# Performance work log

Hardware: AMD Instinct MI355X
Metric: run time of the kernel (lower is better)

## Reference

```python
import jax, jax.numpy as jnp
import numpy as np

B, C, M, NH, F_, W = 2, 8, 8, 8, 1024, 512  # batch, channels, attention_maps, heads, features, frames
HD = F_ // NH
EXP = 4


def _conv(x, w, b):
    y = jax.lax.conv_general_dilated(x, w, (1, 1), 'SAME',
                                     dimension_numbers=('NCHW', 'OIHW', 'NCHW'))
    return y + b[None, :, None, None]


def _rope(x):
    # x: (..., seq, d); lucidrains-style interleaved rotary embedding
    d, n = x.shape[-1], x.shape[-2]
    inv = 1.0 / (10000.0 ** (jnp.arange(0, d, 2, dtype=jnp.float32) / d))
    fr = jnp.repeat(jnp.arange(n, dtype=jnp.float32)[:, None] * inv[None, :], 2, axis=-1)
    cos, sin = jnp.cos(fr), jnp.sin(fr)
    xr = jnp.stack((-x[..., 1::2], x[..., 0::2]), axis=-1).reshape(x.shape)
    return x * cos + xr * sin


def _mcln(x, w, b, eps=1e-5):
    # MultichannelLayerNorm: normalize over features axis (axis=2 of B,C,F,W)
    mu = jnp.mean(x, axis=2, keepdims=True)
    var = jnp.var(x, axis=2, keepdims=True)
    return (x - mu) / jnp.sqrt(var + eps) * w[None, :, :, None] + b[None, :, :, None]


def _mclin(x, w_pw):
    # MultichannelLinear positionwise: per-channel matmul over features
    return jnp.einsum('bcfw,cgf->bcgw', x, w_pw)


def setup_inputs() -> dict:
    key = jax.random.key(0)
    ks = jax.random.split(key, 24)
    s = 0.02
    d = {
        'x': jax.random.normal(ks[0], (B, C, F_, W), jnp.float32),
        'prev_qk': jax.random.normal(ks[1], (B, M, NH, W, W), jnp.float32),
        'qconv_w': jax.random.normal(ks[2], (M, C, 3, 3), jnp.float32) * s,
        'qconv_b': jnp.zeros((M,), jnp.float32),
        'q_pw': jax.random.normal(ks[3], (M, F_, F_), jnp.float32) * s,
        'kconv_w': jax.random.normal(ks[4], (M, C, 3, 3), jnp.float32) * s,
        'kconv_b': jnp.zeros((M,), jnp.float32),
        'k_pw': jax.random.normal(ks[5], (M, F_, F_), jnp.float32) * s,
        'vconv_w': jax.random.normal(ks[6], (M, C, 3, 3), jnp.float32) * s,
        'vconv_b': jnp.zeros((M,), jnp.float32),
        'v_pw': jax.random.normal(ks[7], (M, F_, F_), jnp.float32) * s,
        'o_pw': jax.random.normal(ks[8], (M, F_, F_), jnp.float32) * s,
        'o_dw': jax.random.normal(ks[9], (M, M), jnp.float32) * s,
        'oproj_w': jax.random.normal(ks[10], (C, C + M, 3, 3), jnp.float32) * s,
        'oproj_b': jnp.zeros((C,), jnp.float32),
        'n1_w': jnp.ones((C, F_), jnp.float32),
        'n1_b': jnp.zeros((C, F_), jnp.float32),
        'c1_w': jax.random.normal(ks[11], (C * EXP, C, 3, 3), jnp.float32) * s,
        'c1_b': jnp.zeros((C * EXP,), jnp.float32),
        'c2_w': jax.random.normal(ks[12], (C, C * EXP, 3, 3), jnp.float32) * s,
        'c2_b': jnp.zeros((C,), jnp.float32),
        'n2_w': jnp.ones((C, F_), jnp.float32),
        'n2_b': jnp.zeros((C, F_), jnp.float32),
    }
    return d


def _encoder(x, prev_qk, qconv_w, qconv_b, q_pw, kconv_w, kconv_b, k_pw,
             vconv_w, vconv_b, v_pw, o_pw, o_dw, oproj_w, oproj_b,
             n1_w, n1_b, c1_w, c1_b, c2_w, c2_b, n2_w, n2_b):
    b, c, h, w = x.shape

    def heads(y):  # (B,M,F,W) -> (B,M,NH,W,HD)
        return y.transpose(0, 1, 3, 2).reshape(b, M, w, NH, HD).transpose(0, 1, 3, 2, 4)

    q = _rope(heads(_mclin(_conv(x, qconv_w, qconv_b), q_pw)))
    k = _rope(heads(_mclin(_conv(x, kconv_w, kconv_b), k_pw)))
    v = heads(_mclin(_conv(x, vconv_w, vconv_b), v_pw))

    qk = jnp.einsum('bmnqd,bmnkd->bmnqk', q, k) / jnp.sqrt(jnp.float32(h))
    qk = qk + prev_qk
    a = jnp.einsum('bmnqk,bmnkd->bmnqd', jax.nn.softmax(qk, axis=-1), v)
    a = a.transpose(0, 1, 3, 2, 4).reshape(b, M, w, NH * HD).transpose(0, 1, 3, 2)  # (B,M,F,W)
    a = jnp.einsum('bcfw,dc->bdfw', _mclin(a, o_pw), o_dw)  # depthwise o_linear
    z = _conv(jnp.concatenate((x, a), axis=1), oproj_w, oproj_b)

    hid = _mcln(x + z, n1_w, n1_b)  # dropout is identity in eval
    z2 = _conv(jax.nn.gelu(_conv(hid, c1_w, c1_b), approximate=False), c2_w, c2_b)
    out = _mcln(hid + z2, n2_w, n2_b)
    return out, qk


def reference(x, prev_qk, qconv_w, qconv_b, q_pw, kconv_w, kconv_b, k_pw,
              vconv_w, vconv_b, v_pw, o_pw, o_dw, oproj_w, oproj_b,
              n1_w, n1_b, c1_w, c1_b, c2_w, c2_b, n2_w, n2_b):
    out, qk = _encoder(x, prev_qk, qconv_w, qconv_b, q_pw, kconv_w, kconv_b, k_pw,
                       vconv_w, vconv_b, v_pw, o_pw, o_dw, oproj_w, oproj_b,
                       n1_w, n1_b, c1_w, c1_b, c2_w, c2_b, n2_w, n2_b)
    return (out, out, qk)
```

## Files before the change

### kernel.cpp

```cpp
#include <hip/hip_runtime.h>
#include <math.h>

#define B_ 2
#define C_ 8
#define M_ 8
#define NH_ 8
#define F_ 1024
#define W_ 512
#define HD_ 128
#define FW 524288L
#define PF_ 1026
#define PW_ 514

typedef __bf16 bf16_t;
typedef __bf16 bf16x8 __attribute__((ext_vector_type(8)));
typedef __bf16 bf16x4 __attribute__((ext_vector_type(4)));
typedef float f32x4 __attribute__((ext_vector_type(4)));

__device__ __forceinline__ void gload16(const void* g, void* l) {
    __builtin_amdgcn_global_load_lds(
        (const __attribute__((address_space(1))) unsigned int*)g,
        (__attribute__((address_space(3))) unsigned int*)l,
        16, 0, 0);
}

__device__ __forceinline__ float gelu_f(float v) {
    return 0.5f * v * (1.0f + erff(v * 0.70710678118f));
}

__device__ __forceinline__ void xcd_swz3(int& bx, int& by, int& bz) {
    const int nwg = gridDim.x * gridDim.y * gridDim.z;
    int orig = blockIdx.x + gridDim.x * (blockIdx.y + gridDim.y * blockIdx.z);
    orig = (orig & 7) * (nwg >> 3) + (orig >> 3);
    bx = orig % gridDim.x;
    int t = orig / gridDim.x;
    by = t % gridDim.y;
    bz = t / gridDim.y;
}

__global__ __launch_bounds__(256)
void prep_k(const float* __restrict__ q_pw, const float* __restrict__ k_pw,
            const float* __restrict__ v_pw, const float* __restrict__ o_pw,
            const float* __restrict__ x,
            const float* __restrict__ qw, const float* __restrict__ kw,
            const float* __restrict__ vw, const float* __restrict__ ow,
            const float* __restrict__ c1w, const float* __restrict__ c2w,
            const float* __restrict__ qb, const float* __restrict__ kb,
            const float* __restrict__ vb,
            bf16_t* __restrict__ W4, bf16_t* __restrict__ px,
            bf16_t* __restrict__ a_qkv, bf16_t* __restrict__ a_op,
            bf16_t* __restrict__ a_c1, bf16_t* __restrict__ a_c2,
            float* __restrict__ bias_qkv,
            bf16_t* __restrict__ p8a, bf16_t* __restrict__ p8b, bf16_t* __restrict__ p32)
{
    const int bid = blockIdx.x, tid = threadIdx.x;
    if (bid < 32768) {
        long i = (long)bid * 256 + tid;
        const int wsel = (int)(i >> 21);
        const long off = i & 2097151L;
        const float* src = (wsel == 0) ? q_pw : (wsel == 1) ? k_pw : (wsel == 2) ? v_pw : o_pw;
        float4 v = ((const float4*)src)[off];
        bf16x4 r = { (bf16_t)v.x, (bf16_t)v.y, (bf16_t)v.z, (bf16_t)v.w };
        *(bf16x4*)&W4[i * 4] = r;
    } else if (bid < 36889) {
        long i = (long)(bid - 32768) * 256 + tid;
        if (i >= (long)B_ * PF_ * PW_) return;
        int wc = (int)(i % PW_);
        long t = i / PW_;
        int fr = (int)(t % PF_);
        int b  = (int)(t / PF_);
        bf16x8 v = {};
        if (fr >= 1 && fr <= F_ && wc >= 1 && wc <= W_) {
            const float* s = x + (long)b * 8 * FW + (long)(fr - 1) * W_ + (wc - 1);
            #pragma unroll
            for (int c = 0; c < 8; ++c) v[c] = (bf16_t)s[c * FW];
        }
        *(bf16x8*)&px[i * 8] = v;
    } else if (bid < 36961) {
        int sub = bid - 36889;
        int mode = sub / 18;
        int i = (sub % 18) * 256 + tid;
        if (mode == 0) {
            if (i < 3072) {
                int k = i & 31, co = (i >> 5) & 31, df = i >> 10;
                int tap = k >> 3, ci = k & 7;
                float v = 0.f;
                if (tap < 3) {
                    if (co < 8)       v = qw[((co * 8 + ci) * 3 + df) * 3 + tap];
                    else if (co < 16) v = kw[(((co - 8) * 8 + ci) * 3 + df) * 3 + tap];
                    else if (co < 24) v = vw[(((co - 16) * 8 + ci) * 3 + df) * 3 + tap];
                }
                a_qkv[i] = (bf16_t)v;
            }
            if (i < 32) bias_qkv[i] = (i < 8) ? qb[i] : (i < 16) ? kb[i - 8] : (i < 24) ? vb[i - 16] : 0.f;
        } else if (mode == 1) {
            if (i < 3072) {
                int k = i & 63, co = (i >> 6) & 15, df = i >> 10;
                int src = k >> 5, r = k & 31, tap = r >> 3, ci = src * 8 + (r & 7);
                float v = 0.f;
                if (co < 8 && tap < 3) v = ow[((co * 16 + ci) * 3 + df) * 3 + tap];
                a_op[i] = (bf16_t)v;
            }
        } else if (mode == 2) {
            if (i < 3072) {
                int k = i & 31, co = (i >> 5) & 31, df = i >> 10;
                int tap = k >> 3, ci = k & 7;
                float v = (tap < 3) ? c1w[((co * 8 + ci) * 3 + df) * 3 + tap] : 0.f;
                a_c1[i] = (bf16_t)v;
            }
        } else {
            if (i < 4608) {
                int k = i % 96, co = (i / 96) & 15, df = i / (96 * 16);
                int tap = k >> 5, ci = k & 31;
                float v = (co < 8) ? c2w[((co * 32 + ci) * 3 + df) * 3 + tap] : 0.f;
                a_c2[i] = (bf16_t)v;
            }
        }
    } else {
        int i = (bid - 36961) * 256 + tid;
        if (i >= 2 * 3076) return;
        int b = i / 3076, p = i % 3076;
        int fr, wc;
        if (p < 514)       { fr = 0;    wc = p; }
        else if (p < 1028) { fr = 1025; wc = p - 514; }
        else if (p < 2052) { fr = 1 + (p - 1028); wc = 0; }
        else               { fr = 1 + (p - 2052); wc = 513; }
        long pix = ((long)b * PF_ + fr) * PW_ + wc;
        bf16x8 z = {};
        *(bf16x8*)&p8a[pix * 8] = z;
        *(bf16x8*)&p8b[pix * 8] = z;
        #pragma unroll
        for (int k = 0; k < 4; ++k) *(bf16x8*)&p32[pix * 32 + k * 8] = z;
    }
}

template<int CIN, int KSTEPS, int MFRAGS, int DUAL, int EPI, int RESBF>
__global__ __launch_bounds__(256)
void convg_k(const bf16_t* __restrict__ px0, const bf16_t* __restrict__ px1,
             const bf16_t* __restrict__ Ab, const float* __restrict__ bias,
             const void* __restrict__ resid, void* __restrict__ outp)
{
    const int f = blockIdx.y, b = blockIdx.z;
    const int tid = threadIdx.x, lane = tid & 63, wid = tid >> 6;
    const int l15 = lane & 15, l4 = lane >> 4;
    const int wbase = blockIdx.x * 256 + wid * 64;
    const int KW = KSTEPS * 32, M16 = MFRAGS * 16;

    bf16x8 af[3][MFRAGS][KSTEPS];
    #pragma unroll
    for (int df = 0; df < 3; ++df)
        #pragma unroll
        for (int mf = 0; mf < MFRAGS; ++mf)
            #pragma unroll
            for (int kk = 0; kk < KSTEPS; ++kk)
                af[df][mf][kk] = *(const bf16x8*)&Ab[(long)(df * M16 + mf * 16 + l15) * KW + kk * 32 + l4 * 8];

    f32x4 acc[MFRAGS][4];
    #pragma unroll
    for (int mf = 0; mf < MFRAGS; ++mf)
        #pragma unroll
        for (int nf = 0; nf < 4; ++nf)
            acc[mf][nf] = (f32x4){0.f, 0.f, 0.f, 0.f};

    #pragma unroll
    for (int df = 0; df < 3; ++df) {
        const long rowb = ((long)(b * PF_ + f + df)) * PW_ * CIN;
        #pragma unroll
        for (int nf = 0; nf < 4; ++nf) {
            const int wp = wbase + nf * 16 + l15;
            #pragma unroll
            for (int kk = 0; kk < KSTEPS; ++kk) {
                const bf16_t* src = (DUAL && kk == 1) ? px1 : px0;
                long addr = (CIN == 8) ? rowb + (long)(wp + l4) * 8
                                       : rowb + (long)(wp + kk) * 32 + l4 * 8;
                bf16x8 bv = *(const bf16x8*)&src[addr];
                #pragma unroll
                for (int mf = 0; mf < MFRAGS; ++mf)
                    acc[mf][nf] = __builtin_amdgcn_mfma_f32_16x16x32_bf16(
                        af[df][mf][kk], bv, acc[mf][nf], 0, 0, 0);
            }
        }
    }

    #pragma unroll
    for (int mf = 0; mf < MFRAGS; ++mf) {
        #pragma unroll
        for (int nf = 0; nf < 4; ++nf) {
            const int wp = wbase + nf * 16 + l15;
            if (EPI == 2) {
                const int cob = mf * 16 + l4 * 4;
                bf16x4 ov;
                #pragma unroll
                for (int r = 0; r < 4; ++r)
                    ov[r] = (bf16_t)gelu_f(acc[mf][nf][r] + bias[cob + r]);
                *(bf16x4*)&((bf16_t*)outp)[(((long)(b * PF_ + f + 1)) * PW_ + wp + 1) * 32 + cob] = ov;
            } else {
                #pragma unroll
                for (int r = 0; r < 4; ++r) {
                    const int co = mf * 16 + l4 * 4 + r;
                    float v = acc[mf][nf][r];
                    if (EPI == 0) {
                        if (co < 24)
                            ((bf16_t*)outp)[((long)(b * 24 + co)) * FW + (long)f * W_ + wp] = (bf16_t)(v + bias[co]);
                    } else {
                        if (co < 8) {
                            long oi = ((long)(b * 8 + co)) * FW + (long)f * W_ + wp;
                            float rv = RESBF ? (float)((const bf16_t*)resid)[oi]
                                             : ((const float*)resid)[oi];
                            ((bf16_t*)outp)[oi] = (bf16_t)(v + bias[co] + rv);
                        }
                    }
                }
            }
        }
    }
}

template<int OUTBF>
__global__ __launch_bounds__(256, 4)
void gemm_mfma_k(const bf16_t* __restrict__ Ab, const bf16_t* __restrict__ Bb,
                 void* __restrict__ Cb,
                 int Kdim, int lda, int ldb, int ldc,
                 long sA, long sB, long sC_hi, long sC_lo, int zdivC, int aMod)
{
    __shared__ bf16_t sAt[8192];
    __shared__ bf16_t sBt[8192];

    int bx, by, bz;
    xcd_swz3(bx, by, bz);
    const int z = bz;
    const int m0 = by * 128;
    const int n0 = bx * 128;
    const int tid = threadIdx.x;
    const int lane = tid & 63, wid = tid >> 6;
    const int wr = (wid >> 1) * 64, wc = (wid & 1) * 64;
    const int l15 = lane & 15, l4 = lane >> 4;

    const bf16_t* A = Ab + (long)(z % aMod) * sA;
    const bf16_t* B = Bb + (long)z * sB;

    f32x4 acc[4][4];
    #pragma unroll
    for (int m = 0; m < 4; ++m)
        #pragma unroll
        for (int n = 0; n < 4; ++n)
            acc[m][n] = (f32x4){0.f, 0.f, 0.f, 0.f};

    const int grow = wid * 8 + (lane >> 3);
    const int gslot = lane & 7;

    for (int k0 = 0; k0 < Kdim; k0 += 64) {
        __syncthreads();
        #pragma unroll
        for (int r = 0; r < 4; ++r) {
            const int row = r * 32 + grow;
            gload16(A + (long)(m0 + row) * lda + k0 + ((gslot ^ (row & 7)) << 3),
                    sAt + r * 2048 + wid * 512);
        }
        #pragma unroll
        for (int r = 0; r < 4; ++r) {
            const int row = r * 32 + grow;
            gload16(B + (long)(n0 + row) * ldb + k0 + ((gslot ^ (row & 7)) << 3),
                    sBt + r * 2048 + wid * 512);
        }
        __syncthreads();

        bf16x8 afr[4][2], bfr[4][2];
        #pragma unroll
        for (int m = 0; m < 4; ++m) {
            const int row = wr + m * 16 + l15, swz = row & 7;
            afr[m][0] = *(const bf16x8*)&sAt[row * 64 + ((l4 ^ swz) << 3)];
            afr[m][1] = *(const bf16x8*)&sAt[row * 64 + (((4 + l4) ^ swz) << 3)];
        }
        #pragma unroll
        for (int n = 0; n < 4; ++n) {
            const int row = wc + n * 16 + l15, swz = row & 7;
            bfr[n][0] = *(const bf16x8*)&sBt[row * 64 + ((l4 ^ swz) << 3)];
            bfr[n][1] = *(const bf16x8*)&sBt[row * 64 + (((4 + l4) ^ swz) << 3)];
        }
        #pragma unroll
        for (int kk = 0; kk < 2; ++kk)
            #pragma unroll
            for (int m = 0; m < 4; ++m)
                #pragma unroll
                for (int n = 0; n < 4; ++n)
                    acc[m][n] = __builtin_amdgcn_mfma_f32_16x16x32_bf16(
                        afr[m][kk], bfr[n][kk], acc[m][n], 0, 0, 0);
    }

    const long zc = (long)(z / zdivC) * sC_hi + (long)(z % zdivC) * sC_lo;
    #pragma unroll
    for (int m = 0; m < 4; ++m) {
        #pragma unroll
        for (int n = 0; n < 4; ++n) {
            #pragma unroll
            for (int r = 0; r < 4; ++r) {
                int row = m0 + wr + m * 16 + l4 * 4 + r;
                int col = n0 + wc + n * 16 + l15;
                float v = acc[m][n][r];
                long cidx = zc + (long)row * ldc + col;
                if (OUTBF) ((bf16_t*)Cb)[cidx] = (bf16_t)v;
                else       ((float*)Cb)[cidx]  = v;
            }
        }
    }
}

__global__ __launch_bounds__(256, 4)
void qkvgemm_k(const bf16_t* __restrict__ W4, const bf16_t* __restrict__ XT,
               bf16_t* __restrict__ outp )
{
    __shared__ bf16_t sAt[8192];
    __shared__ bf16_t sBt[8192];

    int bx, by, bz;
    xcd_swz3(bx, by, bz);
    const int zz = bz;
    const int path = zz >> 4, bm = zz & 15;
    const bf16_t* A = W4 + (long)(path * 8 + (bm & 7)) * 1048576L;
    const bf16_t* B = XT + (long)zz * FW;
    const int m0 = by * 128;
    const int n0 = bx * 128;
    const int tid = threadIdx.x;
    const int lane = tid & 63, wid = tid >> 6;
    const int wr = (wid >> 1) * 64, wc = (wid & 1) * 64;
    const int l15 = lane & 15, l4 = lane >> 4;

    f32x4 acc[4][4];
    #pragma unroll
    for (int m = 0; m < 4; ++m)
        #pragma unroll
        for (int n = 0; n < 4; ++n)
            acc[m][n] = (f32x4){0.f, 0.f, 0.f, 0.f};

    const int grow = wid * 8 + (lane >> 3);
    const int gslot = lane & 7;

    for (int k0 = 0; k0 < 1024; k0 += 64) {
        __syncthreads();
        #pragma unroll
        for (int r = 0; r < 4; ++r) {
            const int row = r * 32 + grow;
            gload16(A + (long)(m0 + row) * 1024 + k0 + ((gslot ^ (row & 7)) << 3),
                    sAt + r * 2048 + wid * 512);
        }
        #pragma unroll
        for (int r = 0; r < 4; ++r) {
            const int row = r * 32 + grow;
            gload16(B + (long)(n0 + row) * 1024 + k0 + ((gslot ^ (row & 7)) << 3),
                    sBt + r * 2048 + wid * 512);
        }
        __syncthreads();

        bf16x8 afr[4][2], bfr[4][2];
        #pragma unroll
        for (int m = 0; m < 4; ++m) {
            const int row = wr + m * 16 + l15, swz = row & 7;
            afr[m][0] = *(const bf16x8*)&sAt[row * 64 + ((l4 ^ swz) << 3)];
            afr[m][1] = *(const bf16x8*)&sAt[row * 64 + (((4 + l4) ^ swz) << 3)];
        }
        #pragma unroll
        for (int n = 0; n < 4; ++n) {
            const int row = wc + n * 16 + l15, swz = row & 7;
            bfr[n][0] = *(const bf16x8*)&sBt[row * 64 + ((l4 ^ swz) << 3)];
            bfr[n][1] = *(const bf16x8*)&sBt[row * 64 + (((4 + l4) ^ swz) << 3)];
        }
        #pragma unroll
        for (int kk = 0; kk < 2; ++kk)
            #pragma unroll
            for (int m = 0; m < 4; ++m)
                #pragma unroll
                for (int n = 0; n < 4; ++n)
                    acc[m][n] = __builtin_amdgcn_mfma_f32_16x16x32_bf16(
                        afr[m][kk], bfr[n][kk], acc[m][n], 0, 0, 0);
    }

    if (path < 2) {
        const long base = (long)path * 8388608L + (((long)bm * 8 + by) * 512L) * 128L;
        #pragma unroll
        for (int m = 0; m < 4; ++m) {
            const int d0 = wr + m * 16 + l4 * 4;
            const float inv0 = __expf(-(float)(d0 >> 1) * 0.14391156507f);
            const float inv1 = __expf(-(float)((d0 >> 1) + 1) * 0.14391156507f);
            #pragma unroll
            for (int n = 0; n < 4; ++n) {
                const int col = n0 + wc + n * 16 + l15;
                float s0, c0, s1, c1;
                __sincosf((float)col * inv0, &s0, &c0);
                __sincosf((float)col * inv1, &s1, &c1);
                float v0 = acc[m][n][0], v1 = acc[m][n][1];
                float v2 = acc[m][n][2], v3 = acc[m][n][3];
                bf16x4 ov = { (bf16_t)(v0 * c0 - v1 * s0), (bf16_t)(v1 * c0 + v0 * s0),
                              (bf16_t)(v2 * c1 - v3 * s1), (bf16_t)(v3 * c1 + v2 * s1) };
                *(bf16x4*)&outp[base + (long)col * 128 + d0] = ov;
            }
        }
    } else {
        const long base = 16777216L + (long)bm * FW;
        #pragma unroll
        for (int m = 0; m < 4; ++m)
            #pragma unroll
            for (int n = 0; n < 4; ++n)
                #pragma unroll
                for (int r = 0; r < 4; ++r) {
                    int row = m0 + wr + m * 16 + l4 * 4 + r;
                    int col = n0 + wc + n * 16 + l15;
                    outp[base + (long)row * 512 + col] = (bf16_t)acc[m][n][r];
                }
    }
}

__global__ __launch_bounds__(256, 4)
void attn_k(const bf16_t* __restrict__ QR, const bf16_t* __restrict__ KR,
            const bf16_t* __restrict__ VL, const float* __restrict__ prevb,
            float* __restrict__ Sout, bf16_t* __restrict__ AT)
{
    __shared__ bf16_t sA[4096];
    __shared__ bf16_t sB[8192];
    __shared__ float red[2][64][2];
    __shared__ float Mrun[64], Srun[64];

    int bx, by, bz;
    xcd_swz3(bx, by, bz);
    (void)by;
    const int z = bz;
    const int m0 = bx * 64;
    const bf16_t* Qb = QR + (long)z * 65536L;
    const bf16_t* Kb = KR + (long)z * 65536L;
    const bf16_t* Vb = VL + (long)z * 65536L;
    const float* prev = prevb + (long)z * 262144L;
    float* Sb = Sout + (long)z * 262144L;

    const int tid = threadIdx.x, lane = tid & 63, wid = tid >> 6;
    const int l15 = lane & 15, l4 = lane >> 4;
    const int wr = (wid >> 1) * 32, wc = (wid & 1) * 64;
    const int grow = wid * 8 + (lane >> 3);
    const int gslot = lane & 7;

    if (tid < 64) { Mrun[tid] = -1e30f; Srun[tid] = 0.f; }

    for (int kc = 0; kc < 4; ++kc) {
        f32x4 acc[2][4];
        #pragma unroll
        for (int m = 0; m < 2; ++m)
            #pragma unroll
            for (int n = 0; n < 4; ++n)
                acc[m][n] = (f32x4){0.f, 0.f, 0.f, 0.f};

        #pragma unroll
        for (int k0 = 0; k0 < 128; k0 += 64) {
            __syncthreads();
            #pragma unroll
            for (int r = 0; r < 2; ++r) {
                const int row = r * 32 + grow;
                gload16(Qb + (long)(m0 + row) * 128 + k0 + ((gslot ^ (row & 7)) << 3),
                        sA + r * 2048 + wid * 512);
            }
            #pragma unroll
            for (int r = 0; r < 4; ++r) {
                const int row = r * 32 + grow;
                gload16(Kb + (long)(kc * 128 + row) * 128 + k0 + ((gslot ^ (row & 7)) << 3),
                        sB + r * 2048 + wid * 512);
            }
            __syncthreads();

            bf16x8 afr[2][2], bfr[4][2];
            #pragma unroll
            for (int m = 0; m < 2; ++m) {
                const int row = wr + m * 16 + l15, swz = row & 7;
                afr[m][0] = *(const bf16x8*)&sA[row * 64 + ((l4 ^ swz) << 3)];
                afr[m][1] = *(const bf16x8*)&sA[row * 64 + (((4 + l4) ^ swz) << 3)];
            }
            #pragma unroll
            for (int n = 0; n < 4; ++n) {
                const int row = wc + n * 16 + l15, swz = row & 7;
                bfr[n][0] = *(const bf16x8*)&sB[row * 64 + ((l4 ^ swz) << 3)];
                bfr[n][1] = *(const bf16x8*)&sB[row * 64 + (((4 + l4) ^ swz) << 3)];
            }
            __builtin_amdgcn_s_setprio(1);
            #pragma unroll
            for (int kk = 0; kk < 2; ++kk)
                #pragma unroll
                for (int m = 0; m < 2; ++m)
                    #pragma unroll
                    for (int n = 0; n < 4; ++n)
                        acc[m][n] = __builtin_amdgcn_mfma_f32_16x16x32_bf16(
                            afr[m][kk], bfr[n][kk], acc[m][n], 0, 0, 0);
            __builtin_amdgcn_s_setprio(0);
        }

        #pragma unroll
        for (int m = 0; m < 2; ++m) {
            #pragma unroll
            for (int n = 0; n < 4; ++n) {
                #pragma unroll
                for (int r = 0; r < 4; ++r) {
                    int row = m0 + wr + m * 16 + l4 * 4 + r;
                    int col = kc * 128 + wc + n * 16 + l15;
                    float v = acc[m][n][r] * 0.03125f + prev[(long)row * 512 + col];
                    acc[m][n][r] = v;
                    Sb[(long)row * 512 + col] = v;
                }
            }
        }
        #pragma unroll
        for (int m = 0; m < 2; ++m) {
            #pragma unroll
            for (int r = 0; r < 4; ++r) {
                float mx = -1e30f;
                #pragma unroll
                for (int n = 0; n < 4; ++n) mx = fmaxf(mx, acc[m][n][r]);
                #pragma unroll
                for (int o = 1; o <= 8; o <<= 1) mx = fmaxf(mx, __shfl_xor(mx, o, 64));
                float se = 0.f;
                #pragma unroll
                for (int n = 0; n < 4; ++n) se += __expf(acc[m][n][r] - mx);
                #pragma unroll
                for (int o = 1; o <= 8; o <<= 1) se += __shfl_xor(se, o, 64);
                if (l15 == 0) {
                    int row = wr + m * 16 + l4 * 4 + r;
                    red[wid & 1][row][0] = mx;
                    red[wid & 1][row][1] = se;
                }
            }
        }
        __syncthreads();
        if (tid < 64) {
            float ma = red[0][tid][0], sa = red[0][tid][1];
            float mb = red[1][tid][0], sb = red[1][tid][1];
            float mt = fmaxf(ma, mb);
            float st = sa * __expf(ma - mt) + sb * __expf(mb - mt);
            float M0 = Mrun[tid], S0 = Srun[tid];
            float M1 = fmaxf(M0, mt);
            Srun[tid] = S0 * __expf(M0 - M1) + st * __expf(mt - M1);
            Mrun[tid] = M1;
        }
    }
    __syncthreads();

    f32x4 oacc[2][4];
    #pragma unroll
    for (int m = 0; m < 2; ++m)
        #pragma unroll
        for (int n = 0; n < 4; ++n)
            oacc[m][n] = (f32x4){0.f, 0.f, 0.f, 0.f};

    const int prow0 = tid >> 4, pl = tid & 15;

    for (int kt = 0; kt < 512; kt += 64) {
        __syncthreads();
        #pragma unroll
        for (int p = 0; p < 4; ++p) {
            const int row = p * 16 + prow0;
            float4 v = *(const float4*)(Sb + (long)(m0 + row) * 512 + kt + pl * 4);
            float mr = Mrun[row];
            bf16x4 e = { (bf16_t)__expf(v.x - mr), (bf16_t)__expf(v.y - mr),
                         (bf16_t)__expf(v.z - mr), (bf16_t)__expf(v.w - mr) };
            *(bf16x4*)((char*)sA + row * 128 + ((((pl >> 1) ^ (row & 7))) << 4) + (pl & 1) * 8) = e;
        }
        #pragma unroll
        for (int r = 0; r < 4; ++r) {
            const int row = r * 32 + grow;
            gload16(Vb + (long)row * 512 + kt + ((gslot ^ (row & 7)) << 3),
                    sB + r * 2048 + wid * 512);
        }
        __syncthreads();

        bf16x8 afr[2][2], bfr[4][2];
        #pragma unroll
        for (int m = 0; m < 2; ++m) {
            const int row = wr + m * 16 + l15, swz = row & 7;
            afr[m][0] = *(const bf16x8*)&sA[row * 64 + ((l4 ^ swz) << 3)];
            afr[m][1] = *(const bf16x8*)&sA[row * 64 + (((4 + l4) ^ swz) << 3)];
        }
        #pragma unroll
        for (int n = 0; n < 4; ++n) {
            const int row = wc + n * 16 + l15, swz = row & 7;
            bfr[n][0] = *(const bf16x8*)&sB[row * 64 + ((l4 ^ swz) << 3)];
            bfr[n][1] = *(const bf16x8*)&sB[row * 64 + (((4 + l4) ^ swz) << 3)];
        }
        __builtin_amdgcn_s_setprio(1);
        #pragma unroll
        for (int kk = 0; kk < 2; ++kk)
            #pragma unroll
            for (int m = 0; m < 2; ++m)
                #pragma unroll
                for (int n = 0; n < 4; ++n)
                    oacc[m][n] = __builtin_amdgcn_mfma_f32_16x16x32_bf16(
                        afr[m][kk], bfr[n][kk], oacc[m][n], 0, 0, 0);
        __builtin_amdgcn_s_setprio(0);
    }

    const long base = (long)(z >> 3) * FW + (long)(z & 7) * 128L;
    #pragma unroll
    for (int m = 0; m < 2; ++m) {
        #pragma unroll
        for (int n = 0; n < 4; ++n) {
            #pragma unroll
            for (int r = 0; r < 4; ++r) {
                const int row = wr + m * 16 + l4 * 4 + r;
                const int col = wc + n * 16 + l15;
                float v = oacc[m][n][r] / Srun[row];
                AT[base + (long)(m0 + row) * 1024 + col] = (bf16_t)v;
            }
        }
    }
}

__global__ __launch_bounds__(256)
void tcvt_k(const bf16_t* __restrict__ in, bf16_t* __restrict__ outp)
{
    __shared__ float tile[32][33];
    const int w0 = blockIdx.x * 32, f0 = blockIdx.y * 32;
    const int z = blockIdx.z;
    const int path = z >> 4, bm = z & 15;
    const int inSlice = (bm >> 3) * 24 + path * 8 + (bm & 7);
    const long ibase = (long)inSlice * FW;
    const long obase = (long)z * FW;
    const int tx = threadIdx.x & 31, ty = threadIdx.x >> 5;
    #pragma unroll
    for (int i = 0; i < 4; ++i)
        tile[ty + i * 8][tx] = (float)in[ibase + (long)(f0 + ty + i * 8) * W_ + w0 + tx];
    __syncthreads();
    #pragma unroll
    for (int i = 0; i < 4; ++i)
        outp[obase + (long)(w0 + ty + i * 8) * F_ + f0 + tx] = (bf16_t)tile[tx][ty + i * 8];
}

__global__ __launch_bounds__(256)
void odw_k(const bf16_t* __restrict__ t, const float* __restrict__ dw, bf16_t* __restrict__ px)
{
    long i = (long)blockIdx.x * 256 + threadIdx.x;
    int w = (int)(i & (W_ - 1));
    long q = i >> 9;
    int f = (int)(q & (F_ - 1));
    int b = (int)(q >> 10);
    const bf16_t* s = t + (long)b * 8 * FW + (long)f * W_ + w;
    float tv[8];
    #pragma unroll
    for (int c = 0; c < 8; ++c) tv[c] = (float)s[c * FW];
    bf16x8 o;
    #pragma unroll
    for (int d = 0; d < 8; ++d) {
        float a = 0.f;
        #pragma unroll
        for (int c = 0; c < 8; ++c) a += tv[c] * dw[d * 8 + c];
        o[d] = (bf16_t)a;
    }
    *(bf16x8*)&px[(((long)b * PF_ + f + 1) * PW_ + w + 1) * 8] = o;
}

template<typename TIN, int O1BF>
__global__ __launch_bounds__(256)
void mcln_k(const TIN* __restrict__ in, const float* __restrict__ gam,
            const float* __restrict__ bet, void* __restrict__ o1, float* __restrict__ o2,
            bf16_t* __restrict__ px)
{
    int wi = threadIdx.x & 31, fg = threadIdx.x >> 5;
    int w0 = blockIdx.x * 32;
    int c = blockIdx.y, b = blockIdx.z;
    long base = ((long)b * C_ + c) * FW + w0 + wi;
    float s = 0.f, q = 0.f;
    for (int f = fg; f < F_; f += 8) {
        float v = (float)in[base + (long)f * W_];
        s += v; q += v * v;
    }
    __shared__ float rs[8][33], rq[8][33];
    __shared__ float mu_s[32], inv_s[32];
    rs[fg][wi] = s; rq[fg][wi] = q;
    __syncthreads();
    if (fg == 0) {
        float ts = 0.f, tq = 0.f;
        for (int g = 0; g < 8; ++g) { ts += rs[g][wi]; tq += rq[g][wi]; }
        float mu = ts * (1.0f / F_);
        float var = tq * (1.0f / F_) - mu * mu;
        mu_s[wi] = mu;
        inv_s[wi] = rsqrtf(var + 1e-5f);
    }
    __syncthreads();
    float mu = mu_s[wi], inv = inv_s[wi];
    for (int f = fg; f < F_; f += 8) {
        float v = (float)in[base + (long)f * W_];
        float r = (v - mu) * inv * gam[c * F_ + f] + bet[c * F_ + f];
        long oi = base + (long)f * W_;
        if (O1BF) ((bf16_t*)o1)[oi] = (bf16_t)r;
        else      ((float*)o1)[oi]  = r;
        if (o2) o2[oi] = r;
        if (px) px[(((long)b * PF_ + f + 1) * PW_ + (w0 + wi) + 1) * 8 + c] = (bf16_t)r;
    }
}

extern "C" void kernel_launch(void* const* d_in, const int* in_sizes, int n_in,
                              void* d_out, int out_size, void* d_ws, size_t ws_size,
                              hipStream_t stream) {
    (void)in_sizes; (void)n_in; (void)out_size; (void)ws_size;
    const float* x        = (const float*)d_in[0];
    const float* prev_qk  = (const float*)d_in[1];
    const float* qconv_w  = (const float*)d_in[2];
    const float* qconv_b  = (const float*)d_in[3];
    const float* q_pw     = (const float*)d_in[4];
    const float* kconv_w  = (const float*)d_in[5];
    const float* kconv_b  = (const float*)d_in[6];
    const float* k_pw     = (const float*)d_in[7];
    const float* vconv_w  = (const float*)d_in[8];
    const float* vconv_b  = (const float*)d_in[9];
    const float* v_pw     = (const float*)d_in[10];
    const float* o_pw     = (const float*)d_in[11];
    const float* o_dw     = (const float*)d_in[12];
    const float* oproj_w  = (const float*)d_in[13];
    const float* oproj_b  = (const float*)d_in[14];
    const float* n1_w     = (const float*)d_in[15];
    const float* n1_b     = (const float*)d_in[16];
    const float* c1_w     = (const float*)d_in[17];
    const float* c1_b     = (const float*)d_in[18];
    const float* c2_w     = (const float*)d_in[19];
    const float* c2_b     = (const float*)d_in[20];
    const float* n2_w     = (const float*)d_in[21];
    const float* n2_b     = (const float*)d_in[22];

    float* out    = (float*)d_out;
    float* qk_out = out + 16777216L;

    char* wsb = (char*)d_ws;
    bf16_t* PX8  = (bf16_t*)(wsb + 0L);
    bf16_t* W4   = (bf16_t*)(wsb + 16876032L);
    bf16_t* QR   = (bf16_t*)(wsb + 83984896L);
    bf16_t* KR   = (bf16_t*)(wsb + 100762112L);
    bf16_t* VL   = (bf16_t*)(wsb + 117539328L);
    bf16_t* XT48 = (bf16_t*)(wsb + 134316544L);
    bf16_t* HIDb = (bf16_t*)(wsb + 134316544L);
    bf16_t* QKV  = (bf16_t*)(wsb + 184648192L);
    bf16_t* AT   = (bf16_t*)(wsb + 184648192L);
    bf16_t* F1b  = (bf16_t*)(wsb + 201425408L);
    bf16_t* PRE  = (bf16_t*)(wsb + 218202624L);
    bf16_t* PXA2 = (bf16_t*)(wsb + 234979840L);
    bf16_t* PXH  = (bf16_t*)(wsb + 251855616L);
    bf16_t* PXC1 = (bf16_t*)(wsb + 268731392L);
    bf16_t* ABQ  = (bf16_t*)(wsb + 336233984L);
    bf16_t* ABO  = (bf16_t*)(wsb + 336233984L + 16384L);
    bf16_t* ABC1 = (bf16_t*)(wsb + 336233984L + 32768L);
    bf16_t* ABC2 = (bf16_t*)(wsb + 336233984L + 49152L);
    float*  BQKV = (float*) (wsb + 336233984L + 65536L);

    const dim3 cvgrid(2, F_, B_);
    const dim3 tgrid(16, 32, 48);

    prep_k<<<36986, 256, 0, stream>>>(q_pw, k_pw, v_pw, o_pw, x,
                                      qconv_w, kconv_w, vconv_w, oproj_w, c1_w, c2_w,
                                      qconv_b, kconv_b, vconv_b,
                                      W4, PX8, ABQ, ABO, ABC1, ABC2, BQKV,
                                      PXA2, PXH, PXC1);

    convg_k<8, 1, 2, 0, 0, 0><<<cvgrid, 256, 0, stream>>>(PX8, nullptr, ABQ, BQKV, nullptr, QKV);

    tcvt_k<<<tgrid, 256, 0, stream>>>(QKV, XT48);
    qkvgemm_k<<<dim3(4, 8, 48), 256, 0, stream>>>(W4, XT48, QR);

    attn_k<<<dim3(8, 1, 128), 256, 0, stream>>>(QR, KR, VL, prev_qk, qk_out, AT);

    gemm_mfma_k<1><<<dim3(4, 8, 16), 256, 0, stream>>>(W4 + 25165824L, AT, F1b,
        F_, F_, F_, W_, 1048576L, 524288L, 524288L, 0L, 1, 8);
    odw_k<<<4096, 256, 0, stream>>>(F1b, o_dw, PXA2);

    convg_k<8, 2, 1, 1, 1, 0><<<cvgrid, 256, 0, stream>>>(PX8, PXA2, ABO, oproj_b, x, PRE);

    mcln_k<bf16_t, 1><<<dim3(16, 8, 2), 256, 0, stream>>>(PRE, n1_w, n1_b, HIDb, nullptr, PXH);

    convg_k<8, 1, 2, 0, 2, 0><<<cvgrid, 256, 0, stream>>>(PXH, nullptr, ABC1, c1_b, nullptr, PXC1);
    convg_k<32, 3, 1, 0, 1, 1><<<cvgrid, 256, 0, stream>>>(PXC1, nullptr, ABC2, c2_b, HIDb, PRE);
    mcln_k<bf16_t, 0><<<dim3(16, 8, 2), 256, 0, stream>>>(PRE, n2_w, n2_b, out, out + 8388608L, nullptr);
}
```

Baseline: 611.0 us.

## Register-prefetch Q/K/V tiles to overlap global loads with MFMA in attention

Replaces the direct global-to-LDS loads in the attention kernel's QK and PV loops with register prefetch. Each iteration stores the already-loaded tile from registers into LDS, then issues the next tile's global loads before computing. The two nested QK loops are flattened into one 8-step loop, and the PV loop computes the exp values before the barrier. The aim is to hide global load latency behind MFMA work, at the cost of extra VGPRs and explicit LDS stores.

```diff
diff --git a/kernel.cpp b/kernel.cpp
--- a/kernel.cpp
+++ b/kernel.cpp
@@ -439,101 +439,122 @@
 
     if (tid < 64) { Mrun[tid] = -1e30f; Srun[tid] = 0.f; }
 
-    for (int kc = 0; kc < 4; ++kc) {
-        f32x4 acc[2][4];
-        #pragma unroll
-        for (int m = 0; m < 2; ++m)
-            #pragma unroll
-            for (int n = 0; n < 4; ++n)
-                acc[m][n] = (f32x4){0.f, 0.f, 0.f, 0.f};
-
-        #pragma unroll
-        for (int k0 = 0; k0 < 128; k0 += 64) {
+    bf16x8 qpre[2], kpre[4];
+    #pragma unroll
+    for (int r = 0; r < 2; ++r)
+        qpre[r] = *(const bf16x8*)&Qb[(long)(m0 + r * 32 + grow) * 128 + gslot * 8];
+    #pragma unroll
+    for (int r = 0; r < 4; ++r)
+        kpre[r] = *(const bf16x8*)&Kb[(long)(r * 32 + grow) * 128 + gslot * 8];
+
+    f32x4 acc[2][4];
+    #pragma unroll
+    for (int m = 0; m < 2; ++m)
+        #pragma unroll
+        for (int n = 0; n < 4; ++n)
+            acc[m][n] = (f32x4){0.f, 0.f, 0.f, 0.f};
+
+    for (int s = 0; s < 8; ++s) {
+        __syncthreads();
+        #pragma unroll
+        for (int r = 0; r < 2; ++r) {
+            const int row = r * 32 + grow;
+            *(bf16x8*)&sA[row * 64 + ((gslot ^ (row & 7)) << 3)] = qpre[r];
+        }
+        #pragma unroll
+        for (int r = 0; r < 4; ++r) {
+            const int row = r * 32 + grow;
+            *(bf16x8*)&sB[row * 64 + ((gslot ^ (row & 7)) << 3)] = kpre[r];
+        }
+        if (s < 7) {
+            const int ns = s + 1;
+            const int nkc = ns >> 1, nk0 = (ns & 1) * 64;
+            #pragma unroll
+            for (int r = 0; r < 2; ++r)
+                qpre[r] = *(const bf16x8*)&Qb[(long)(m0 + r * 32 + grow) * 128 + nk0 + gslot * 8];
+            #pragma unroll
+            for (int r = 0; r < 4; ++r)
+                kpre[r] = *(const bf16x8*)&Kb[(long)(nkc * 128 + r * 32 + grow) * 128 + nk0 + gslot * 8];
+        }
+        __syncthreads();
+
+        bf16x8 afr[2][2], bfr[4][2];
+        #pragma unroll
+        for (int m = 0; m < 2; ++m) {
+            const int row = wr + m * 16 + l15, swz = row & 7;
+            afr[m][0] = *(const bf16x8*)&sA[row * 64 + ((l4 ^ swz) << 3)];
+            afr[m][1] = *(const bf16x8*)&sA[row * 64 + (((4 + l4) ^ swz) << 3)];
+        }
+        #pragma unroll
+        for (int n = 0; n < 4; ++n) {
+            const int row = wc + n * 16 + l15, swz = row & 7;
+            bfr[n][0] = *(const bf16x8*)&sB[row * 64 + ((l4 ^ swz) << 3)];
+            bfr[n][1] = *(const bf16x8*)&sB[row * 64 + (((4 + l4) ^ swz) << 3)];
+        }
+        __builtin_amdgcn_s_setprio(1);
+        #pragma unroll
+        for (int kk = 0; kk < 2; ++kk)
+            #pragma unroll
+            for (int m = 0; m < 2; ++m)
+                #pragma unroll
+                for (int n = 0; n < 4; ++n)
+                    acc[m][n] = __builtin_amdgcn_mfma_f32_16x16x32_bf16(
+                        afr[m][kk], bfr[n][kk], acc[m][n], 0, 0, 0);
+        __builtin_amdgcn_s_setprio(0);
+
+        if (s & 1) {
+            const int kc = s >> 1;
+            #pragma unroll
+            for (int m = 0; m < 2; ++m) {
+                #pragma unroll
+                for (int n = 0; n < 4; ++n) {
+                    #pragma unroll
+                    for (int r = 0; r < 4; ++r) {
+                        int row = m0 + wr + m * 16 + l4 * 4 + r;
+                        int col = kc * 128 + wc + n * 16 + l15;
+                        float v = acc[m][n][r] * 0.03125f + prev[(long)row * 512 + col];
+                        acc[m][n][r] = v;
+                        Sb[(long)row * 512 + col] = v;
+                    }
+                }
+            }
+            #pragma unroll
+            for (int m = 0; m < 2; ++m) {
+                #pragma unroll
+                for (int r = 0; r < 4; ++r) {
+                    float mx = -1e30f;
+                    #pragma unroll
+                    for (int n = 0; n < 4; ++n) mx = fmaxf(mx, acc[m][n][r]);
+                    #pragma unroll
+                    for (int o = 1; o <= 8; o <<= 1) mx = fmaxf(mx, __shfl_xor(mx, o, 64));
+                    float se = 0.f;
+                    #pragma unroll
+                    for (int n = 0; n < 4; ++n) se += __expf(acc[m][n][r] - mx);
+                    #pragma unroll
+                    for (int o = 1; o <= 8; o <<= 1) se += __shfl_xor(se, o, 64);
+                    if (l15 == 0) {
+                        int row = wr + m * 16 + l4 * 4 + r;
+                        red[wid & 1][row][0] = mx;
+                        red[wid & 1][row][1] = se;
+                    }
+                }
+            }
             __syncthreads();
-            #pragma unroll
-            for (int r = 0; r < 2; ++r) {
-                const int row = r * 32 + grow;
-                gload16(Qb + (long)(m0 + row) * 128 + k0 + ((gslot ^ (row & 7)) << 3),
-                        sA + r * 2048 + wid * 512);
-            }
-            #pragma unroll
-            for (int r = 0; r < 4; ++r) {
-                const int row = r * 32 + grow;
-                gload16(Kb + (long)(kc * 128 + row) * 128 + k0 + ((gslot ^ (row & 7)) << 3),
-                        sB + r * 2048 + wid * 512);
-            }
-            __syncthreads();
-
-            bf16x8 afr[2][2], bfr[4][2];
-            #pragma unroll
-            for (int m = 0; m < 2; ++m) {
-                const int row = wr + m * 16 + l15, swz = row & 7;
-                afr[m][0] = *(const bf16x8*)&sA[row * 64 + ((l4 ^ swz) << 3)];
-                afr[m][1] = *(const bf16x8*)&sA[row * 64 + (((4 + l4) ^ swz) << 3)];
-            }
-            #pragma unroll
-            for (int n = 0; n < 4; ++n) {
-                const int row = wc + n * 16 + l15, swz = row & 7;
-                bfr[n][0] = *(const bf16x8*)&sB[row * 64 + ((l4 ^ swz) << 3)];
-                bfr[n][1] = *(const bf16x8*)&sB[row * 64 + (((4 + l4) ^ swz) << 3)];
-            }
-            __builtin_amdgcn_s_setprio(1);
-            #pragma unroll
-            for (int kk = 0; kk < 2; ++kk)
-                #pragma unroll
-                for (int m = 0; m < 2; ++m)
-                    #pragma unroll
-                    for (int n = 0; n < 4; ++n)
-                        acc[m][n] = __builtin_amdgcn_mfma_f32_16x16x32_bf16(
-                            afr[m][kk], bfr[n][kk], acc[m][n], 0, 0, 0);
-            __builtin_amdgcn_s_setprio(0);
-        }
-
-        #pragma unroll
-        for (int m = 0; m < 2; ++m) {
-            #pragma unroll
-            for (int n = 0; n < 4; ++n) {
-                #pragma unroll
-                for (int r = 0; r < 4; ++r) {
-                    int row = m0 + wr + m * 16 + l4 * 4 + r;
-                    int col = kc * 128 + wc + n * 16 + l15;
-                    float v = acc[m][n][r] * 0.03125f + prev[(long)row * 512 + col];
-                    acc[m][n][r] = v;
-                    Sb[(long)row * 512 + col] = v;
-                }
-            }
-        }
-        #pragma unroll
-        for (int m = 0; m < 2; ++m) {
-            #pragma unroll
-            for (int r = 0; r < 4; ++r) {
-                float mx = -1e30f;
-                #pragma unroll
-                for (int n = 0; n < 4; ++n) mx = fmaxf(mx, acc[m][n][r]);
-                #pragma unroll
-                for (int o = 1; o <= 8; o <<= 1) mx = fmaxf(mx, __shfl_xor(mx, o, 64));
-                float se = 0.f;
-                #pragma unroll
-                for (int n = 0; n < 4; ++n) se += __expf(acc[m][n][r] - mx);
-                #pragma unroll
-                for (int o = 1; o <= 8; o <<= 1) se += __shfl_xor(se, o, 64);
-                if (l15 == 0) {
-                    int row = wr + m * 16 + l4 * 4 + r;
-                    red[wid & 1][row][0] = mx;
-                    red[wid & 1][row][1] = se;
-                }
-            }
-        }
-        __syncthreads();
-        if (tid < 64) {
-            float ma = red[0][tid][0], sa = red[0][tid][1];
-            float mb = red[1][tid][0], sb = red[1][tid][1];
-            float mt = fmaxf(ma, mb);
-            float st = sa * __expf(ma - mt) + sb * __expf(mb - mt);
-            float M0 = Mrun[tid], S0 = Srun[tid];
-            float M1 = fmaxf(M0, mt);
-            Srun[tid] = S0 * __expf(M0 - M1) + st * __expf(mt - M1);
-            Mrun[tid] = M1;
+            if (tid < 64) {
+                float ma = red[0][tid][0], sa = red[0][tid][1];
+                float mb = red[1][tid][0], sb = red[1][tid][1];
+                float mt = fmaxf(ma, mb);
+                float st = sa * __expf(ma - mt) + sb * __expf(mb - mt);
+                float M0 = Mrun[tid], S0 = Srun[tid];
+                float M1 = fmaxf(M0, mt);
+                Srun[tid] = S0 * __expf(M0 - M1) + st * __expf(mt - M1);
+                Mrun[tid] = M1;
+            }
+            #pragma unroll
+            for (int m = 0; m < 2; ++m)
+                #pragma unroll
+                for (int n = 0; n < 4; ++n)
+                    acc[m][n] = (f32x4){0.f, 0.f, 0.f, 0.f};
         }
     }
     __syncthreads();
@@ -547,22 +568,38 @@
 
     const int prow0 = tid >> 4, pl = tid & 15;
 
-    for (int kt = 0; kt < 512; kt += 64) {
-        __syncthreads();
+    bf16x8 vpre[4];
+    #pragma unroll
+    for (int r = 0; r < 4; ++r)
+        vpre[r] = *(const bf16x8*)&Vb[(long)(r * 32 + grow) * 512 + gslot * 8];
+
+    for (int t = 0; t < 8; ++t) {
+        const int kt = t * 64;
+        bf16x4 e[4];
         #pragma unroll
         for (int p = 0; p < 4; ++p) {
             const int row = p * 16 + prow0;
             float4 v = *(const float4*)(Sb + (long)(m0 + row) * 512 + kt + pl * 4);
             float mr = Mrun[row];
-            bf16x4 e = { (bf16_t)__expf(v.x - mr), (bf16_t)__expf(v.y - mr),
-                         (bf16_t)__expf(v.z - mr), (bf16_t)__expf(v.w - mr) };
-            *(bf16x4*)((char*)sA + row * 128 + ((((pl >> 1) ^ (row & 7))) << 4) + (pl & 1) * 8) = e;
+            e[p] = (bf16x4){ (bf16_t)__expf(v.x - mr), (bf16_t)__expf(v.y - mr),
+                             (bf16_t)__expf(v.z - mr), (bf16_t)__expf(v.w - mr) };
+        }
+        __syncthreads();
+        #pragma unroll
+        for (int p = 0; p < 4; ++p) {
+            const int row = p * 16 + prow0;
+            *(bf16x4*)((char*)sA + row * 128 + ((((pl >> 1) ^ (row & 7))) << 4) + (pl & 1) * 8) = e[p];
         }
         #pragma unroll
         for (int r = 0; r < 4; ++r) {
             const int row = r * 32 + grow;
-            gload16(Vb + (long)row * 512 + kt + ((gslot ^ (row & 7)) << 3),
-                    sB + r * 2048 + wid * 512);
+            *(bf16x8*)&sB[row * 64 + ((gslot ^ (row & 7)) << 3)] = vpre[r];
+        }
+        if (t < 7) {
+            const int nkt = kt + 64;
+            #pragma unroll
+            for (int r = 0; r < 4; ++r)
+                vpre[r] = *(const bf16x8*)&Vb[(long)(r * 32 + grow) * 512 + nkt + gslot * 8];
         }
         __syncthreads();
 
```

Result: slower. 668.6 us (+9.4%).
